# Kernel optimization log

Hardware: AMD Instinct MI355X
Metric: run time of the kernel (lower is better)

The kernel has to match this reference:

```python
import jax, jax.numpy as jnp
import numpy as np

B, P, ENC = 64, 196, 2048
ATT, DEC, EMB = 512, 512, 512
V, MAXLEN = 10000, 30


def setup_inputs() -> dict:
    key = jax.random.key(0)
    ks = jax.random.split(key, 20)
    s = 0.02
    inp = {
        "encoder_out": jax.random.normal(ks[0], (B, P, ENC), jnp.float32),
        "captions": jax.random.randint(ks[1], (B, MAXLEN), 0, V).astype(jnp.int64),
        "caption_lengths": jax.random.randint(ks[2], (B,), 1, MAXLEN).astype(jnp.int64),
        # parameters (PyTorch Linear convention: y = x @ W.T + b)
        "emb_table": jax.random.uniform(ks[3], (V, EMB), jnp.float32, -0.1, 0.1),
        "W_enc_att": jax.random.normal(ks[4], (ATT, ENC), jnp.float32) * s,
        "b_enc_att": jnp.zeros((ATT,), jnp.float32),
        "W_dec_att": jax.random.normal(ks[5], (ATT, DEC), jnp.float32) * s,
        "b_dec_att": jnp.zeros((ATT,), jnp.float32),
        "w_full_att": jax.random.normal(ks[6], (1, ATT), jnp.float32) * s,
        "b_full_att": jnp.zeros((1,), jnp.float32),
        "W_ih": jax.random.normal(ks[7], (4 * DEC, EMB + ENC), jnp.float32) * s,
        "b_ih": jnp.zeros((4 * DEC,), jnp.float32),
        "W_hh": jax.random.normal(ks[8], (4 * DEC, DEC), jnp.float32) * s,
        "b_hh": jnp.zeros((4 * DEC,), jnp.float32),
        "W_init_h": jax.random.normal(ks[9], (DEC, ENC), jnp.float32) * s,
        "b_init_h": jnp.zeros((DEC,), jnp.float32),
        "W_init_c": jax.random.normal(ks[10], (DEC, ENC), jnp.float32) * s,
        "b_init_c": jnp.zeros((DEC,), jnp.float32),
        "W_fc": jax.random.uniform(ks[11], (V, DEC), jnp.float32, -0.1, 0.1),
        "b_fc": jnp.zeros((V,), jnp.float32),
    }
    return inp


def reference(encoder_out, captions, caption_lengths, emb_table,
              W_enc_att, b_enc_att, W_dec_att, b_dec_att,
              w_full_att, b_full_att, W_ih, b_ih, W_hh, b_hh,
              W_init_h, b_init_h, W_init_c, b_init_c, W_fc, b_fc):
    # init hidden state from mean-pooled encoder features
    mean_enc = encoder_out.mean(axis=1)                       # [B, ENC]
    h0 = mean_enc @ W_init_h.T + b_init_h                     # [B, DEC]
    c0 = mean_enc @ W_init_c.T + b_init_c                     # [B, DEC]

    # encoder-side attention projection is time-invariant: hoist out of the loop
    att1 = jnp.einsum('bpe,ae->bpa', encoder_out, W_enc_att) + b_enc_att  # [B, P, ATT]

    embeddings = emb_table[captions]                          # [B, T, EMB]
    T = captions.shape[1] - 1
    emb_steps = jnp.swapaxes(embeddings[:, :T, :], 0, 1)      # [T, B, EMB]

    def step(carry, emb_t):
        h, c = carry
        att2 = h @ W_dec_att.T + b_dec_att                    # [B, ATT]
        e = (jax.nn.relu(att1 + att2[:, None, :]) @ w_full_att.T + b_full_att)[..., 0]  # [B, P]
        alpha = jax.nn.softmax(e, axis=1)                     # [B, P]
        context = jnp.einsum('bp,bpe->be', alpha, encoder_out)  # [B, ENC]
        x = jnp.concatenate([emb_t, context], axis=1)         # [B, EMB+ENC]
        gates = x @ W_ih.T + b_ih + h @ W_hh.T + b_hh         # [B, 4*DEC]
        i, f, g, o = jnp.split(gates, 4, axis=1)
        c_new = jax.nn.sigmoid(f) * c + jax.nn.sigmoid(i) * jnp.tanh(g)
        h_new = jax.nn.sigmoid(o) * jnp.tanh(c_new)
        preds = h_new @ W_fc.T + b_fc                         # dropout in eval mode = identity
        return (h_new, c_new), (preds, alpha)

    _, (preds_seq, alpha_seq) = jax.lax.scan(step, (h0, c0), emb_steps)
    predictions = jnp.swapaxes(preds_seq, 0, 1)               # [B, T, V]
    alphas = jnp.swapaxes(alpha_seq, 0, 1)                    # [B, T, P]
    return predictions, alphas
```

## Files before the change

kernel.cpp:

```cpp
#include <hip/hip_runtime.h>
#include <cstddef>

constexpr int B_   = 64;
constexpr int P_   = 196;
constexpr int ENC_ = 2048;
constexpr int ATT_ = 512;
constexpr int DEC_ = 512;
constexpr int EMB_ = 512;
constexpr int V_   = 10000;
constexpr int MAXLEN_ = 30;
constexpr int T_   = 29;
constexpr int G4_  = 2048;
constexpr int KIH_ = 2560;
constexpr int XK2_ = 2560;

constexpr int NBLK = 256;
constexpr int TPB  = 1024;
constexpr int NT   = NBLK * TPB;
constexpr int NW   = NT / 64;
constexpr int FSTR = 16;
constexpr size_t ZS_ = (size_t)B_ * G4_;
constexpr int NPT = 625;

typedef __attribute__((ext_vector_type(8))) short short8;
typedef __attribute__((ext_vector_type(4))) float f32x4;
using us = unsigned short;

__device__ __forceinline__ us f2bf(float x) {
    union { float f; unsigned u; } v; v.f = x;
    unsigned r = v.u + 0x7fff + ((v.u >> 16) & 1);
    return (us)(r >> 16);
}
__device__ __forceinline__ float bf2f(us u) {
    union { unsigned u; float f; } v; v.u = ((unsigned)u) << 16;
    return v.f;
}

__device__ __forceinline__ unsigned ld4cc(const void* p) {
    unsigned r;
    asm volatile("global_load_dword %0, %1, off sc1\n\ts_waitcnt vmcnt(0)"
                 : "=v"(r) : "v"(p) : "memory");
    return r;
}
__device__ __forceinline__ void ld4cc_x8(const float* p0, const float* p1,
                                         const float* p2, const float* p3,
                                         const float* p4, const float* p5,
                                         const float* p6, const float* p7,
                                         float* o) {
    float r0, r1, r2, r3, r4, r5, r6, r7;
    asm volatile("global_load_dword %0, %8, off sc1\n\t"
                 "global_load_dword %1, %9, off sc1\n\t"
                 "global_load_dword %2, %10, off sc1\n\t"
                 "global_load_dword %3, %11, off sc1\n\t"
                 "global_load_dword %4, %12, off sc1\n\t"
                 "global_load_dword %5, %13, off sc1\n\t"
                 "global_load_dword %6, %14, off sc1\n\t"
                 "global_load_dword %7, %15, off sc1\n\t"
                 "s_waitcnt vmcnt(0)"
                 : "=&v"(r0), "=&v"(r1), "=&v"(r2), "=&v"(r3),
                   "=&v"(r4), "=&v"(r5), "=&v"(r6), "=&v"(r7)
                 : "v"(p0), "v"(p1), "v"(p2), "v"(p3),
                   "v"(p4), "v"(p5), "v"(p6), "v"(p7) : "memory");
    o[0]=r0; o[1]=r1; o[2]=r2; o[3]=r3; o[4]=r4; o[5]=r5; o[6]=r6; o[7]=r7;
}
__device__ __forceinline__ void ld16cc_x3(const void* p0, const void* p1, const void* p2,
                                          short8* a, short8* b, short8* c) {
    short8 ra, rb, rc;
    asm volatile("global_load_dwordx4 %0, %3, off sc1\n\t"
                 "global_load_dwordx4 %1, %4, off sc1\n\t"
                 "global_load_dwordx4 %2, %5, off sc1\n\t"
                 "s_waitcnt vmcnt(0)"
                 : "=&v"(ra), "=&v"(rb), "=&v"(rc)
                 : "v"(p0), "v"(p1), "v"(p2) : "memory");
    *a = ra; *b = rb; *c = rc;
}
__device__ __forceinline__ void ld16cc_x4(const void* p0, const void* p1,
                                          const void* p2, const void* p3,
                                          short8* a, short8* b, short8* c, short8* d) {
    short8 ra, rb, rc, rd;
    asm volatile("global_load_dwordx4 %0, %4, off sc1\n\t"
                 "global_load_dwordx4 %1, %5, off sc1\n\t"
                 "global_load_dwordx4 %2, %6, off sc1\n\t"
                 "global_load_dwordx4 %3, %7, off sc1\n\t"
                 "s_waitcnt vmcnt(0)"
                 : "=&v"(ra), "=&v"(rb), "=&v"(rc), "=&v"(rd)
                 : "v"(p0), "v"(p1), "v"(p2), "v"(p3) : "memory");
    *a = ra; *b = rb; *c = rc; *d = rd;
}
__device__ __forceinline__ void ldf8cc(const void* p0, const void* p1, f32x4* a, f32x4* b) {
    f32x4 ra, rb;
    asm volatile("global_load_dwordx4 %0, %2, off sc1\n\t"
                 "global_load_dwordx4 %1, %3, off sc1\n\t"
                 "s_waitcnt vmcnt(0)"
                 : "=&v"(ra), "=&v"(rb) : "v"(p0), "v"(p1) : "memory");
    *a = ra; *b = rb;
}
__device__ __forceinline__ void st4cc(void* p, unsigned v) {
    asm volatile("global_store_dword %0, %1, off sc1" :: "v"(p), "v"(v) : "memory");
}
__device__ __forceinline__ void st2cc(void* p, unsigned v) {
    asm volatile("global_store_short %0, %1, off sc1" :: "v"(p), "v"(v) : "memory");
}
__device__ __forceinline__ float wredsum(float a) {
#pragma unroll
    for (int o = 32; o > 0; o >>= 1) a += __shfl_xor(a, o);
    return a;
}

template<bool REL>
__device__ __forceinline__ void gbar_arrive(unsigned* flags, unsigned tok) {
    asm volatile("s_waitcnt vmcnt(0)" ::: "memory");
    __syncthreads();
    if (threadIdx.x == 0)
        __hip_atomic_store(&flags[blockIdx.x * FSTR], tok,
                           REL ? __ATOMIC_RELEASE : __ATOMIC_RELAXED,
                           __HIP_MEMORY_SCOPE_AGENT);
}
__device__ __forceinline__ void gbar_wait(unsigned* flags, unsigned tok) {
    if (threadIdx.x < NBLK) {
        while (__hip_atomic_load(&flags[threadIdx.x * FSTR], __ATOMIC_RELAXED,
                                 __HIP_MEMORY_SCOPE_AGENT) < tok)
            __builtin_amdgcn_s_sleep(1);
    }
    __syncthreads();
}
template<bool REL>
__device__ __forceinline__ void gbar(unsigned* flags, unsigned tok) {
    gbar_arrive<REL>(flags, tok);
    gbar_wait(flags, tok);
}

__device__ __forceinline__ void cvt8(const float* __restrict__ src, us* __restrict__ dst) {
    const float4* p = (const float4*)src;
    float4 a = p[0], b = p[1];
    union { short8 v; us u[8]; } o;
    o.u[0] = f2bf(a.x); o.u[1] = f2bf(a.y); o.u[2] = f2bf(a.z); o.u[3] = f2bf(a.w);
    o.u[4] = f2bf(b.x); o.u[5] = f2bf(b.y); o.u[6] = f2bf(b.z); o.u[7] = f2bf(b.w);
    *(short8*)dst = o.v;
}

__device__ __forceinline__ float score8(short8 v, const f32x4& lo, const f32x4& hi,
                                        const float4& w0, const float4& w1) {
    float acc = 0.f, x;
    x = bf2f((us)v[0]) + lo[0]; acc += fmaxf(x, 0.f) * w0.x;
    x = bf2f((us)v[1]) + lo[1]; acc += fmaxf(x, 0.f) * w0.y;
    x = bf2f((us)v[2]) + lo[2]; acc += fmaxf(x, 0.f) * w0.z;
    x = bf2f((us)v[3]) + lo[3]; acc += fmaxf(x, 0.f) * w0.w;
    x = bf2f((us)v[4]) + hi[0]; acc += fmaxf(x, 0.f) * w1.x;
    x = bf2f((us)v[5]) + hi[1]; acc += fmaxf(x, 0.f) * w1.y;
    x = bf2f((us)v[6]) + hi[2]; acc += fmaxf(x, 0.f) * w1.z;
    x = bf2f((us)v[7]) + hi[3]; acc += fmaxf(x, 0.f) * w1.w;
    return acc;
}

__device__ __forceinline__ void preds_task(const us* s_h, const us* __restrict__ wfcb,
                                           const float* __restrict__ b_fc,
                                           float* __restrict__ outp,
                                           int nt, int tt, int lane) {
    const int r = lane & 15, g = lane >> 4;
    f32x4 acc[4] = {{0,0,0,0},{0,0,0,0},{0,0,0,0},{0,0,0,0}};
    const us* Brow = wfcb + (size_t)(nt*16 + r)*DEC_ + g*8;
    const us* As   = s_h + r*520 + g*8;
#pragma unroll
    for (int k0 = 0; k0 < DEC_; k0 += 64) {
        short8 b0 = *(const short8*)(Brow + k0);
        short8 b1 = *(const short8*)(Brow + k0 + 32);
#pragma unroll
        for (int mt = 0; mt < 4; ++mt) {
            short8 a0 = *(const short8*)(As + mt*16*520 + k0);
            short8 a1 = *(const short8*)(As + mt*16*520 + k0 + 32);
            acc[mt] = __builtin_amdgcn_mfma_f32_16x16x32_bf16(a0, b0, acc[mt], 0, 0, 0);
            acc[mt] = __builtin_amdgcn_mfma_f32_16x16x32_bf16(a1, b1, acc[mt], 0, 0, 0);
        }
    }
    const int n = nt*16 + r;
    const float bv = b_fc[n];
#pragma unroll
    for (int mt = 0; mt < 4; ++mt)
#pragma unroll
        for (int i = 0; i < 4; ++i) {
            int b = mt*16 + g*4 + i;
            outp[(size_t)b*(T_*V_) + (size_t)tt*V_ + n] = acc[mt][i] + bv;
        }
}

__global__ __launch_bounds__(TPB)
void k_persist(
    const float* __restrict__ enc, const int* __restrict__ captions,
    const float* __restrict__ emb_table,
    const float* __restrict__ W_enc_att, const float* __restrict__ b_enc_att,
    const float* __restrict__ W_dec_att, const float* __restrict__ b_dec_att,
    const float* __restrict__ w_full,
    const float* __restrict__ W_ih, const float* __restrict__ b_ih,
    const float* __restrict__ W_hh, const float* __restrict__ b_hh,
    const float* __restrict__ W_init_h, const float* __restrict__ b_init_h,
    const float* __restrict__ W_init_c, const float* __restrict__ b_init_c,
    const float* __restrict__ W_fc, const float* __restrict__ b_fc,
    us* encb, us* wencb, us* wdecb, us* wfcb, us* wcat2, us* wembW,
    us* winitb, us* xembA, us* att1b, us* hbuf, us* xcatb, us* meanbb,
    float* cst, float* att2G, float* gp, float* gpe, float* bsum,
    unsigned* flags, float* outp, float* outa)
{
    __shared__ us s_stage[64 * 520];
    __shared__ us s_wb[64 * 328];
    __shared__ us s_wd[16 * 520];
    __shared__ float s_e[P_];
    __shared__ float s_al[P_];
    __shared__ float s_red[32];

    const int tid = threadIdx.x, bid = blockIdx.x;
    const int gtid = bid * TPB + tid;
    const int wid  = gtid >> 6;
    const int w    = tid >> 6;
    const int lane = tid & 63;
    unsigned tok = 0;
    float creg = 0.f;
    us* const hb0 = hbuf;
    us* const hb1 = hbuf + (size_t)B_ * DEC_;
    unsigned* const aflags = flags + (NBLK + 16) * FSTR;

    for (int i = gtid; i < B_*P_*ENC_/8; i += NT) cvt8(enc + (size_t)i*8, encb + (size_t)i*8);
    for (int i = gtid; i < ATT_*ENC_/8; i += NT) cvt8(W_enc_att + (size_t)i*8, wencb + (size_t)i*8);
    for (int i = gtid; i < ATT_*DEC_/8; i += NT) cvt8(W_dec_att + (size_t)i*8, wdecb + (size_t)i*8);
    for (int i = gtid; i < V_*DEC_/8;   i += NT) cvt8(W_fc + (size_t)i*8, wfcb + (size_t)i*8);
    for (int i = gtid; i < G4_*XK2_/8;  i += NT) {
        int n = (i*8) / XK2_, k = (i*8) % XK2_;
        const float* src = (k < ENC_) ? (W_ih + (size_t)n*KIH_ + EMB_ + k)
                                      : (W_hh + (size_t)n*DEC_ + (k - ENC_));
        cvt8(src, wcat2 + (size_t)i*8);
    }
    for (int i = gtid; i < G4_*EMB_/8;  i += NT)
        cvt8(W_ih + ((size_t)((i*8) / EMB_))*KIH_ + ((i*8) % EMB_), wembW + (size_t)i*8);
    for (int i = gtid; i < 1024*ENC_/8; i += NT) {
        int n = (i*8) >> 11, k = (i*8) & (ENC_ - 1);
        const float* src = (n < 512) ? (W_init_h + (size_t)n*ENC_ + k)
                                     : (W_init_c + (size_t)(n-512)*ENC_ + k);
        cvt8(src, winitb + (size_t)i*8);
    }
    for (int i = gtid; i < T_*B_*EMB_/8; i += NT) {
        int r = i >> 6, c8 = i & 63;
        int t = r >> 6, b = r & 63;
        int cap = captions[b*MAXLEN_ + t];
        cvt8(emb_table + (size_t)cap*EMB_ + c8*8, xembA + (size_t)r*EMB_ + c8*8);
    }
    if (gtid < G4_) bsum[gtid] = b_ih[gtid] + b_hh[gtid];
    if (gtid < B_*ENC_) {
        int b = gtid >> 11, e = gtid & (ENC_ - 1);
        const float* base = enc + (size_t)b*P_*ENC_ + e;
        float s = 0.f;
        for (int p = 0; p < P_; ++p) s += base[(size_t)p*ENC_];
        meanbb[gtid] = f2bf(s * (1.f / P_));
    }
    gbar<true>(flags, ++tok);

    for (int task = wid; task < 256 + 1856; task += NW) {
        const int r = lane & 15, g = lane >> 4;
        if (task < 256) {
            const int mt = task & 3, nt = task >> 2;
            const int m0 = mt*16, n0 = nt*16;
            const us* Ar = meanbb + (size_t)(m0 + r)*ENC_ + g*8;
            const us* Br = winitb + (size_t)(n0 + r)*ENC_ + g*8;
            f32x4 acc0 = {0,0,0,0}, acc1 = {0,0,0,0};
#pragma unroll 4
            for (int k0 = 0; k0 < ENC_; k0 += 64) {
                acc0 = __builtin_amdgcn_mfma_f32_16x16x32_bf16(
                    *(const short8*)(Ar + k0), *(const short8*)(Br + k0), acc0, 0, 0, 0);
                acc1 = __builtin_amdgcn_mfma_f32_16x16x32_bf16(
                    *(const short8*)(Ar + k0 + 32), *(const short8*)(Br + k0 + 32), acc1, 0, 0, 0);
            }
            const int n = n0 + r;
            if (n < 512) {
                float bv = b_init_h[n];
#pragma unroll
                for (int i = 0; i < 4; ++i) {
                    int b = m0 + g*4 + i;
                    unsigned hv = f2bf(acc0[i] + acc1[i] + bv);
                    st2cc(hb1 + b*DEC_ + n, hv);
                    st2cc(xcatb + (size_t)b*XK2_ + ENC_ + n, hv);
                }
            } else {
                int d = n - 512;
                float bv = b_init_c[d];
#pragma unroll
                for (int i = 0; i < 4; ++i)
                    st4cc(cst + (m0 + g*4 + i)*DEC_ + d,
                          __float_as_uint(acc0[i] + acc1[i] + bv));
            }
        } else {
            const int q = task - 256;
            const int m0 = (q >> 6) * 64, n0 = (q & 63) * 32;
            f32x4 acc[4][2] = {};
            const us* Ab = xembA + (size_t)(m0 + r)*EMB_ + g*8;
            const us* Bb = wembW + (size_t)(n0 + r)*EMB_ + g*8;
#pragma unroll 2
            for (int k0 = 0; k0 < EMB_; k0 += 32) {
                short8 af[4], bfr[2];
#pragma unroll
                for (int mi = 0; mi < 4; ++mi)
                    af[mi] = *(const short8*)(Ab + (size_t)mi*16*EMB_ + k0);
#pragma unroll
                for (int nj = 0; nj < 2; ++nj)
                    bfr[nj] = *(const short8*)(Bb + (size_t)nj*16*EMB_ + k0);
#pragma unroll
                for (int mi = 0; mi < 4; ++mi)
#pragma unroll
                    for (int nj = 0; nj < 2; ++nj)
                        acc[mi][nj] = __builtin_amdgcn_mfma_f32_16x16x32_bf16(
                            af[mi], bfr[nj], acc[mi][nj], 0, 0, 0);
            }
#pragma unroll
            for (int mi = 0; mi < 4; ++mi)
#pragma unroll
                for (int nj = 0; nj < 2; ++nj) {
                    int n = n0 + nj*16 + r;
                    float bv = bsum[n];
#pragma unroll
                    for (int i = 0; i < 4; ++i) {
                        int m = m0 + mi*16 + g*4 + i;
                        gpe[(size_t)m*G4_ + n] = acc[mi][nj][i] + bv;
                    }
                }
        }
    }
    gbar<true>(flags, ++tok);

    for (int task = wid; task < 3264; task += NW) {
        const int r = lane & 15, g = lane >> 4;
        if (task < 3136) {
            int mt = task >> 4, nt2 = task & 15;
            int m0 = mt*64, n0 = nt2*32;
            f32x4 acc[4][2] = {};
            const us* Ab = encb + (size_t)(m0 + r)*ENC_ + g*8;
            const us* Bb = wencb + (size_t)(n0 + r)*ENC_ + g*8;
#pragma unroll 2
            for (int k0 = 0; k0 < ENC_; k0 += 32) {
                short8 af[4], bfr[2];
#pragma unroll
                for (int mi = 0; mi < 4; ++mi)
                    af[mi] = *(const short8*)(Ab + (size_t)mi*16*ENC_ + k0);
#pragma unroll
                for (int nj = 0; nj < 2; ++nj)
                    bfr[nj] = *(const short8*)(Bb + (size_t)nj*16*ENC_ + k0);
#pragma unroll
                for (int mi = 0; mi < 4; ++mi)
#pragma unroll
                    for (int nj = 0; nj < 2; ++nj)
                        acc[mi][nj] = __builtin_amdgcn_mfma_f32_16x16x32_bf16(
                            af[mi], bfr[nj], acc[mi][nj], 0, 0, 0);
            }
#pragma unroll
            for (int mi = 0; mi < 4; ++mi)
#pragma unroll
                for (int nj = 0; nj < 2; ++nj) {
                    int n = n0 + nj*16 + r;
                    float bv = b_enc_att[n];
#pragma unroll
                    for (int i = 0; i < 4; ++i) {
                        int m = m0 + mi*16 + g*4 + i;
                        att1b[(size_t)m*ATT_ + n] = f2bf(acc[mi][nj][i] + bv);
                    }
                }
        } else {
            int q = task - 3136;
            int nt = q >> 2, mt = q & 3;
            const us* Ar = hb1 + (size_t)(mt*16 + r)*DEC_ + g*8;
            const us* Br = wdecb + (size_t)(nt*16 + r)*DEC_ + g*8;
            f32x4 acc0 = {0,0,0,0}, acc1 = {0,0,0,0};
#pragma unroll 4
            for (int k0 = 0; k0 < DEC_; k0 += 64) {
                short8 a0, a1, dum;
                ld16cc_x3(Ar + k0, Ar + k0 + 32, Ar + k0, &a0, &a1, &dum);
                acc0 = __builtin_amdgcn_mfma_f32_16x16x32_bf16(
                    a0, *(const short8*)(Br + k0), acc0, 0, 0, 0);
                acc1 = __builtin_amdgcn_mfma_f32_16x16x32_bf16(
                    a1, *(const short8*)(Br + k0 + 32), acc1, 0, 0, 0);
            }
            int n = nt*16 + r;
            float bv = b_dec_att[n];
#pragma unroll
            for (int i = 0; i < 4; ++i)
                st4cc(att2G + (size_t)(mt*16 + g*4 + i)*ATT_ + n,
                      __float_as_uint(acc0[i] + acc1[i] + bv));
        }
    }
    gbar<true>(flags, ++tok);

    {
        const int z = bid >> 5, nb = bid & 31;
        for (int c = tid; c < 2560; c += TPB) {
            int row = c / 40, col8 = c % 40;
            *(short8*)(s_wb + row*328 + col8*8) =
                *(const short8*)(wcat2 + (size_t)(nb*64 + row)*XK2_ + (size_t)z*320 + col8*8);
        }
        if (bid < 32)
            for (int c = tid; c < 1024; c += TPB) {
                int row = c >> 6, col8 = c & 63;
                *(short8*)(s_wd + row*520 + col8*8) =
                    *(const short8*)(wdecb + (size_t)(bid*16 + row)*DEC_ + col8*8);
            }
        if (tid < 128) creg = __uint_as_float(ld4cc(cst + bid*128 + tid));
        __syncthreads();
    }
    const float4 w0v = *(const float4*)(w_full + lane*8);
    const float4 w1v = *(const float4*)(w_full + lane*8 + 4);

    for (int t = 0; t < T_; ++t) {
        {
            if (t > 0) {
                if (tid < 32) {
                    while (__hip_atomic_load(&aflags[tid * FSTR], __ATOMIC_RELAXED,
                                             __HIP_MEMORY_SCOPE_AGENT) < (unsigned)t)
                        __builtin_amdgcn_s_sleep(1);
                }
                __syncthreads();
            }
            const int b = bid & 63, cc = bid >> 6;
            f32x4 a2lo, a2hi;
            const float* ap = att2G + (size_t)b*ATT_ + lane*8;
            ldf8cc(ap, ap + 4, &a2lo, &a2hi);
            const us* a1base = att1b + (size_t)b*P_*ATT_ + lane*8;
            for (int p = w; p < P_; p += 32) {
                const int p2 = p + 16;
                short8 v0 = *(const short8*)(a1base + (size_t)p*ATT_);
                short8 v1 = (p2 < P_) ? *(const short8*)(a1base + (size_t)p2*ATT_) : v0;
                float acc0 = score8(v0, a2lo, a2hi, w0v, w1v);
                float acc1 = score8(v1, a2lo, a2hi, w0v, w1v);
                acc0 = wredsum(acc0);
                acc1 = wredsum(acc1);
                if (lane == 0) {
                    s_e[p] = acc0;
                    if (p2 < P_) s_e[p2] = acc1;
                }
            }
            __syncthreads();
            float v = (tid < P_) ? s_e[tid] : -3.4e38f;
            float mx = v;
#pragma unroll
            for (int o = 32; o > 0; o >>= 1) mx = fmaxf(mx, __shfl_xor(mx, o));
            if (lane == 0) s_red[w] = mx;
            __syncthreads();
            mx = s_red[0];
#pragma unroll
            for (int j = 1; j < 16; ++j) mx = fmaxf(mx, s_red[j]);
            float ev = (tid < P_) ? expf(v - mx) : 0.f;
            float sm = wredsum(ev);
            if (lane == 0) s_red[16 + w] = sm;
            __syncthreads();
            float tot = 0.f;
#pragma unroll
            for (int j = 0; j < 16; ++j) tot += s_red[16 + j];
            if (tid < P_) {
                float al = ev / tot;
                s_al[tid] = al;
                if (cc == 0) outa[((size_t)b*T_ + t)*P_ + tid] = al;
            }
            __syncthreads();
            float a[8] = {};
            const us* ep = encb + (size_t)b*P_*ENC_ + cc*512 + lane*8;
            for (int p = w; p < P_; p += 16) {
                short8 vv = *(const short8*)(ep + (size_t)p*ENC_);
                float al = s_al[p];
#pragma unroll
                for (int j = 0; j < 8; ++j) a[j] += al * bf2f((us)vv[j]);
            }
            float* s_accf = (float*)s_stage;
            {
                f32x4 lo = {a[0],a[1],a[2],a[3]}, hi = {a[4],a[5],a[6],a[7]};
                *(f32x4*)(s_accf + w*512 + lane*8)     = lo;
                *(f32x4*)(s_accf + w*512 + lane*8 + 4) = hi;
            }
            __syncthreads();
            if (tid < 256) {
                int c2 = tid*2;
                float s0 = 0.f, s1 = 0.f;
#pragma unroll
                for (int q = 0; q < 16; ++q) {
                    s0 += s_accf[q*512 + c2];
                    s1 += s_accf[q*512 + c2 + 1];
                }
                unsigned pk = (unsigned)f2bf(s0) | ((unsigned)f2bf(s1) << 16);
                st4cc(xcatb + (size_t)b*XK2_ + cc*512 + c2, pk);
            }
            __syncthreads();
        }
        gbar<false>(flags, ++tok);

        {
            const int z = bid >> 5;
            {
                short8 v0, v1, v2;
                int c0 = tid, c1 = tid + 1024, c2i = tid + 2048;
                const us* p0 = xcatb + (size_t)(c0/40)*XK2_ + z*320 + (c0%40)*8;
                const us* p1 = xcatb + (size_t)(c1/40)*XK2_ + z*320 + (c1%40)*8;
                bool has2 = c2i < 2560;
                const us* p2 = has2 ? xcatb + (size_t)(c2i/40)*XK2_ + z*320 + (c2i%40)*8 : p0;
                ld16cc_x3(p0, p1, p2, &v0, &v1, &v2);
                *(short8*)(s_stage + (c0/40)*328 + (c0%40)*8) = v0;
                *(short8*)(s_stage + (c1/40)*328 + (c1%40)*8) = v1;
                if (has2) *(short8*)(s_stage + (c2i/40)*328 + (c2i%40)*8) = v2;
            }
            __syncthreads();
            const int nt = (bid & 31)*4 + (w >> 2), mt = w & 3;
            const int r = lane & 15, g = lane >> 4;
            const us* sxr = s_stage + (mt*16 + r)*328 + g*8;
            const us* Br  = s_wb + ((w >> 2)*16 + r)*328 + g*8;
            f32x4 acc0 = {0,0,0,0}, acc1 = {0,0,0,0};
#pragma unroll
            for (int k0 = 0; k0 < 320; k0 += 64) {
                acc0 = __builtin_amdgcn_mfma_f32_16x16x32_bf16(
                    *(const short8*)(sxr + k0), *(const short8*)(Br + k0), acc0, 0, 0, 0);
                acc1 = __builtin_amdgcn_mfma_f32_16x16x32_bf16(
                    *(const short8*)(sxr + k0 + 32), *(const short8*)(Br + k0 + 32), acc1, 0, 0, 0);
            }
            const int n = nt*16 + r;
#pragma unroll
            for (int i = 0; i < 4; ++i) {
                int m = mt*16 + g*4 + i;
                st4cc(gp + ZS_*z + (size_t)m*G4_ + n, __float_as_uint(acc0[i] + acc1[i]));
            }
            __syncthreads();
        }
        gbar<false>(flags, ++tok);

        {
            float* sg = (float*)s_stage;
            if (tid < 512) {
                const int cell = tid & 127, gate = tid >> 7;
                const int idx = bid*128 + cell;
                const int b = idx >> 9, d = idx & 511;
                const float* gz = gp + (size_t)b*G4_ + gate*512 + d;
                float vz[8];
                ld4cc_x8(gz, gz + ZS_, gz + 2*ZS_, gz + 3*ZS_,
                         gz + 4*ZS_, gz + 5*ZS_, gz + 6*ZS_, gz + 7*ZS_, vz);
                sg[tid] = ((vz[0]+vz[1]) + (vz[2]+vz[3])) + ((vz[4]+vz[5]) + (vz[6]+vz[7]));
            }
            __syncthreads();
            if (tid < 128) {
                const int idx = bid*128 + tid;
                const int b = idx >> 9, d = idx & 511;
                const float* ge = gpe + ((size_t)(t*B_ + b))*G4_ + d;
                float gi = sg[tid]       + ge[0];
                float gf = sg[128 + tid] + ge[512];
                float gg = sg[256 + tid] + ge[1024];
                float go = sg[384 + tid] + ge[1536];
                float si = 1.f / (1.f + expf(-gi));
                float sf = 1.f / (1.f + expf(-gf));
                float so = 1.f / (1.f + expf(-go));
                float cn = sf * creg + si * tanhf(gg);
                creg = cn;
                float hn = so * tanhf(cn);
                unsigned hv = f2bf(hn);
                us* hnew = (t & 1) ? hb1 : hb0;
                st2cc(hnew + idx, hv);
                st2cc(xcatb + (size_t)b*XK2_ + ENC_ + d, hv);
            }
        }
        gbar<false>(flags, ++tok);

        if (bid < 32) {
            if (t != T_ - 1) {
                const us* hbn = (t & 1) ? hb1 : hb0;
                short8 v0, v1, v2, v3;
                int c0 = tid, c1 = tid + 1024, c2i = tid + 2048, c3 = tid + 3072;
                ld16cc_x4(hbn + (c0>>6)*DEC_ + (c0&63)*8, hbn + (c1>>6)*DEC_ + (c1&63)*8,
                          hbn + (c2i>>6)*DEC_ + (c2i&63)*8, hbn + (c3>>6)*DEC_ + (c3&63)*8,
                          &v0, &v1, &v2, &v3);
                *(short8*)(s_stage + (c0>>6)*520 + (c0&63)*8) = v0;
                *(short8*)(s_stage + (c1>>6)*520 + (c1&63)*8) = v1;
                *(short8*)(s_stage + (c2i>>6)*520 + (c2i&63)*8) = v2;
                *(short8*)(s_stage + (c3>>6)*520 + (c3&63)*8) = v3;
                __syncthreads();
                if (w < 4) {
                    const int r = lane & 15, g = lane >> 4;
                    const us* As = s_stage + (w*16 + r)*520 + g*8;
                    const us* Bs = s_wd + r*520 + g*8;
                    f32x4 acc0 = {0,0,0,0}, acc1 = {0,0,0,0};
#pragma unroll
                    for (int k0 = 0; k0 < DEC_; k0 += 64) {
                        acc0 = __builtin_amdgcn_mfma_f32_16x16x32_bf16(
                            *(const short8*)(As + k0), *(const short8*)(Bs + k0), acc0, 0, 0, 0);
                        acc1 = __builtin_amdgcn_mfma_f32_16x16x32_bf16(
                            *(const short8*)(As + k0 + 32), *(const short8*)(Bs + k0 + 32), acc1, 0, 0, 0);
                    }
                    const int n = bid*16 + r;
                    float bv = b_dec_att[n];
#pragma unroll
                    for (int i = 0; i < 4; ++i)
                        st4cc(att2G + (size_t)(w*16 + g*4 + i)*ATT_ + n,
                              __float_as_uint(acc0[i] + acc1[i] + bv));
                }
                asm volatile("s_waitcnt vmcnt(0)" ::: "memory");
                __syncthreads();
                if (tid == 0)
                    __hip_atomic_store(&aflags[bid * FSTR], (unsigned)(t + 1),
                                       __ATOMIC_RELAXED, __HIP_MEMORY_SCOPE_AGENT);
            }
        } else if (t > 0) {
            const us* hbo = (t & 1) ? hb0 : hb1;
            short8 v0, v1, v2, v3;
            int c0 = tid, c1 = tid + 1024, c2i = tid + 2048, c3 = tid + 3072;
            ld16cc_x4(hbo + (c0>>6)*DEC_ + (c0&63)*8, hbo + (c1>>6)*DEC_ + (c1&63)*8,
                      hbo + (c2i>>6)*DEC_ + (c2i&63)*8, hbo + (c3>>6)*DEC_ + (c3&63)*8,
                      &v0, &v1, &v2, &v3);
            *(short8*)(s_stage + (c0>>6)*520 + (c0&63)*8) = v0;
            *(short8*)(s_stage + (c1>>6)*520 + (c1&63)*8) = v1;
            *(short8*)(s_stage + (c2i>>6)*520 + (c2i&63)*8) = v2;
            *(short8*)(s_stage + (c3>>6)*520 + (c3&63)*8) = v3;
            __syncthreads();
            const int tq = (bid - 32)*3 + w;
            if (w < 3 && tq < NPT)
                preds_task(s_stage, wfcb, b_fc, outp, tq, t - 1, lane);
            __syncthreads();
        }
    }

    if (bid < 40) {
        __syncthreads();
        const us* hbn = ((T_ - 1) & 1) ? hb1 : hb0;
        {
            short8 v0, v1, v2, v3;
            int c0 = tid, c1 = tid + 1024, c2i = tid + 2048, c3 = tid + 3072;
            ld16cc_x4(hbn + (c0>>6)*DEC_ + (c0&63)*8, hbn + (c1>>6)*DEC_ + (c1&63)*8,
                      hbn + (c2i>>6)*DEC_ + (c2i&63)*8, hbn + (c3>>6)*DEC_ + (c3&63)*8,
                      &v0, &v1, &v2, &v3);
            *(short8*)(s_stage + (c0>>6)*520 + (c0&63)*8) = v0;
            *(short8*)(s_stage + (c1>>6)*520 + (c1&63)*8) = v1;
            *(short8*)(s_stage + (c2i>>6)*520 + (c2i&63)*8) = v2;
            *(short8*)(s_stage + (c3>>6)*520 + (c3&63)*8) = v3;
        }
        __syncthreads();
        const int tq = bid*16 + w;
        if (tq < NPT)
            preds_task(s_stage, wfcb, b_fc, outp, tq, T_ - 1, lane);
    }
}

extern "C" void kernel_launch(void* const* d_in, const int* in_sizes, int n_in,
                              void* d_out, int out_size, void* d_ws, size_t ws_size,
                              hipStream_t stream) {
    const float* enc       = (const float*)d_in[0];
    const int*   captions  = (const int*)d_in[1];
    const float* emb_table = (const float*)d_in[3];
    const float* W_enc_att = (const float*)d_in[4];
    const float* b_enc_att = (const float*)d_in[5];
    const float* W_dec_att = (const float*)d_in[6];
    const float* b_dec_att = (const float*)d_in[7];
    const float* w_full    = (const float*)d_in[8];
    const float* W_ih      = (const float*)d_in[10];
    const float* b_ih      = (const float*)d_in[11];
    const float* W_hh      = (const float*)d_in[12];
    const float* b_hh      = (const float*)d_in[13];
    const float* W_init_h  = (const float*)d_in[14];
    const float* b_init_h  = (const float*)d_in[15];
    const float* W_init_c  = (const float*)d_in[16];
    const float* b_init_c  = (const float*)d_in[17];
    const float* W_fc      = (const float*)d_in[18];
    const float* b_fc      = (const float*)d_in[19];

    char* ws = (char*)d_ws;
    size_t off = 0;
    auto alloc = [&](size_t bytes) {
        void* p = ws + off;
        off = (off + bytes + 255) & ~(size_t)255;
        return p;
    };
    us* encb   = (us*)alloc((size_t)B_ * P_ * ENC_ * 2);
    us* wencb  = (us*)alloc((size_t)ATT_ * ENC_ * 2);
    us* wdecb  = (us*)alloc((size_t)ATT_ * DEC_ * 2);
    us* wfcb   = (us*)alloc((size_t)V_ * DEC_ * 2);
    us* wcat2  = (us*)alloc((size_t)G4_ * XK2_ * 2);
    us* wembW  = (us*)alloc((size_t)G4_ * EMB_ * 2);
    us* winitb = (us*)alloc((size_t)1024 * ENC_ * 2);
    us* xembA  = (us*)alloc((size_t)T_ * B_ * EMB_ * 2);
    us* att1b  = (us*)alloc((size_t)B_ * P_ * ATT_ * 2);
    us* hbuf   = (us*)alloc((size_t)2 * B_ * DEC_ * 2);
    us* xcatb  = (us*)alloc((size_t)B_ * XK2_ * 2);
    us* meanbb = (us*)alloc((size_t)B_ * ENC_ * 2);
    float* cst   = (float*)alloc((size_t)B_ * DEC_ * 4);
    float* att2G = (float*)alloc((size_t)B_ * ATT_ * 4);
    float* gp    = (float*)alloc((size_t)B_ * G4_ * 8 * 4);
    float* gpe   = (float*)alloc((size_t)T_ * B_ * G4_ * 4);
    float* bsum  = (float*)alloc((size_t)G4_ * 4);
    unsigned* flags = (unsigned*)alloc((size_t)(NBLK + 64) * FSTR * 4);

    float* outp = (float*)d_out;
    float* outa = outp + (size_t)B_ * T_ * V_;

    hipMemsetAsync(flags, 0, (NBLK + 64) * FSTR * sizeof(unsigned), stream);
    k_persist<<<NBLK, TPB, 0, stream>>>(
        enc, captions, emb_table, W_enc_att, b_enc_att, W_dec_att, b_dec_att,
        w_full, W_ih, b_ih, W_hh, b_hh, W_init_h, b_init_h, W_init_c, b_init_c,
        W_fc, b_fc,
        encb, wencb, wdecb, wfcb, wcat2, wembW, winitb, xembA, att1b, hbuf, xcatb,
        meanbb, cst, att2G, gp, gpe, bsum, flags, outp, outa);
}
```

Measured before the change: 1.198 ms.

## Double-buffer att1 and encoder row loads into LDS via async global_load_lds

Replaces the direct global loads of att1 rows (score phase) and encoder rows (context phase) with async global-to-LDS loads into two 32-row staging buffers, processed in 7 chunks with explicit vmcnt waits and block barriers. The next chunk is prefetched while the current one is computed, and the first encoder chunk is issued before the softmax to hide its latency. The intent is to overlap memory latency with compute inside the per-step attention. In exchange it adds two barriers per chunk and relies on hand-tuned vmcnt counts, which are fragile if the compiler emits other outstanding loads.

```diff
diff --git a/kernel.cpp b/kernel.cpp
--- a/kernel.cpp
+++ b/kernel.cpp
@@ -26,6 +26,9 @@
 typedef __attribute__((ext_vector_type(4))) float f32x4;
 using us = unsigned short;
 
+typedef __attribute__((address_space(1))) const unsigned int guint;
+typedef __attribute__((address_space(3))) unsigned int luint;
+
 __device__ __forceinline__ us f2bf(float x) {
     union { float f; unsigned u; } v; v.f = x;
     unsigned r = v.u + 0x7fff + ((v.u >> 16) & 1);
@@ -34,6 +37,10 @@
 __device__ __forceinline__ float bf2f(us u) {
     union { unsigned u; float f; } v; v.u = ((unsigned)u) << 16;
     return v.f;
+}
+
+__device__ __forceinline__ void gl_lds16(const us* g, us* l) {
+    __builtin_amdgcn_global_load_lds((guint*)g, (luint*)l, 16, 0, 0);
 }
 
 __device__ __forceinline__ unsigned ld4cc(const void* p) {
@@ -403,6 +410,8 @@
     }
     const float4 w0v = *(const float4*)(w_full + lane*8);
     const float4 w1v = *(const float4*)(w_full + lane*8 + 4);
+    us* const sbuf0 = s_stage;
+    us* const sbuf1 = s_stage + 32*512;
 
     for (int t = 0; t < T_; ++t) {
         {
@@ -419,20 +428,47 @@
             const float* ap = att2G + (size_t)b*ATT_ + lane*8;
             ldf8cc(ap, ap + 4, &a2lo, &a2hi);
             const us* a1base = att1b + (size_t)b*P_*ATT_ + lane*8;
-            for (int p = w; p < P_; p += 32) {
-                const int p2 = p + 16;
-                short8 v0 = *(const short8*)(a1base + (size_t)p*ATT_);
-                short8 v1 = (p2 < P_) ? *(const short8*)(a1base + (size_t)p2*ATT_) : v0;
-                float acc0 = score8(v0, a2lo, a2hi, w0v, w1v);
-                float acc1 = score8(v1, a2lo, a2hi, w0v, w1v);
-                acc0 = wredsum(acc0);
-                acc1 = wredsum(acc1);
-                if (lane == 0) {
-                    s_e[p] = acc0;
-                    if (p2 < P_) s_e[p2] = acc1;
-                }
-            }
-            __syncthreads();
+            const us* epb    = encb + (size_t)b*P_*ENC_ + cc*512 + lane*8;
+
+            {
+                const int rr = w*2;
+                if (rr < 32) {
+                    gl_lds16(a1base + (size_t)(rr    )*ATT_, sbuf0 + (size_t)(rr    )*512);
+                    gl_lds16(a1base + (size_t)(rr + 1)*ATT_, sbuf0 + (size_t)(rr + 1)*512);
+                }
+                for (int c = 0; c < 7; ++c) {
+                    if (c < 6) {
+                        const int r0n = (c + 1)*32, nrn = (c + 1 < 6) ? 32 : 4;
+                        if (rr < nrn) {
+                            us* lb = ((c + 1) & 1) ? sbuf1 : sbuf0;
+                            gl_lds16(a1base + (size_t)(r0n + rr    )*ATT_, lb + (size_t)(rr    )*512);
+                            gl_lds16(a1base + (size_t)(r0n + rr + 1)*ATT_, lb + (size_t)(rr + 1)*512);
+                        }
+                    }
+                    const bool in2 = (c < 5) || (c == 5 && w < 2);
+                    if (in2) asm volatile("s_waitcnt vmcnt(2)" ::: "memory");
+                    else     asm volatile("s_waitcnt vmcnt(0)" ::: "memory");
+                    __syncthreads();
+                    const int r0 = c*32, nr = (c < 6) ? 32 : 4;
+                    if (rr < nr) {
+                        const us* lb = (c & 1) ? sbuf1 : sbuf0;
+#pragma unroll
+                        for (int i = 0; i < 2; ++i) {
+                            short8 v = *(const short8*)(lb + (size_t)(rr + i)*512 + lane*8);
+                            float sc = wredsum(score8(v, a2lo, a2hi, w0v, w1v));
+                            if (lane == 0) s_e[r0 + rr + i] = sc;
+                        }
+                    }
+                    __syncthreads();
+                }
+            }
+            {
+                const int rr = w*2;
+                if (rr < 32) {
+                    gl_lds16(epb + (size_t)(rr    )*ENC_, sbuf0 + (size_t)(rr    )*512);
+                    gl_lds16(epb + (size_t)(rr + 1)*ENC_, sbuf0 + (size_t)(rr + 1)*512);
+                }
+            }
             float v = (tid < P_) ? s_e[tid] : -3.4e38f;
             float mx = v;
 #pragma unroll
@@ -455,13 +491,36 @@
                 if (cc == 0) outa[((size_t)b*T_ + t)*P_ + tid] = al;
             }
             __syncthreads();
+
             float a[8] = {};
-            const us* ep = encb + (size_t)b*P_*ENC_ + cc*512 + lane*8;
-            for (int p = w; p < P_; p += 16) {
-                short8 vv = *(const short8*)(ep + (size_t)p*ENC_);
-                float al = s_al[p];
-#pragma unroll
-                for (int j = 0; j < 8; ++j) a[j] += al * bf2f((us)vv[j]);
+            {
+                const int rr = w*2;
+                for (int c = 0; c < 7; ++c) {
+                    if (c < 6) {
+                        const int r0n = (c + 1)*32, nrn = (c + 1 < 6) ? 32 : 4;
+                        if (rr < nrn) {
+                            us* lb = ((c + 1) & 1) ? sbuf1 : sbuf0;
+                            gl_lds16(epb + (size_t)(r0n + rr    )*ENC_, lb + (size_t)(rr    )*512);
+                            gl_lds16(epb + (size_t)(r0n + rr + 1)*ENC_, lb + (size_t)(rr + 1)*512);
+                        }
+                    }
+                    const bool in2 = (c < 5) || (c == 5 && w < 2);
+                    if (in2) asm volatile("s_waitcnt vmcnt(2)" ::: "memory");
+                    else     asm volatile("s_waitcnt vmcnt(0)" ::: "memory");
+                    __syncthreads();
+                    const int r0 = c*32, nr = (c < 6) ? 32 : 4;
+                    if (rr < nr) {
+                        const us* lb = (c & 1) ? sbuf1 : sbuf0;
+#pragma unroll
+                        for (int i = 0; i < 2; ++i) {
+                            short8 vv = *(const short8*)(lb + (size_t)(rr + i)*512 + lane*8);
+                            const float al = s_al[r0 + rr + i];
+#pragma unroll
+                            for (int k = 0; k < 8; ++k) a[k] += al * bf2f((us)vv[k]);
+                        }
+                    }
+                    __syncthreads();
+                }
             }
             float* s_accf = (float*)s_stage;
             {
```

Result: slower. 1.553 ms (+29.6%).
